# Kernel tuning notes

Hardware: AMD Instinct MI355X
Metric: run time of the kernel (lower is better)

## Reference

```python
import jax, jax.numpy as jnp
import numpy as np

T = 2048        # flattened tokens (one prefill sequence)
HID = 2048      # hidden_size
NH = 32         # query heads
NKV = 4         # kv heads
HD = 128        # head_dim
THETA = 1000000.0
EPS = 1e-6


def setup_inputs() -> dict:
    key = jax.random.key(0)
    k0, k1, k2 = jax.random.split(key, 3)
    return {
        "positions": jnp.arange(T, dtype=jnp.int32),
        "hidden_states": jax.random.normal(k0, (T, HID), dtype=jnp.float32),
        "w_qkv": jax.random.normal(k1, ((NH + 2 * NKV) * HD, HID), dtype=jnp.float32) * 0.02,
        "w_o": jax.random.normal(k2, (HID, NH * HD), dtype=jnp.float32) * 0.02,
        "q_norm_w": jnp.ones((HD,), dtype=jnp.float32),
        "k_norm_w": jnp.ones((HD,), dtype=jnp.float32),
    }


def _rmsnorm(x, w):
    # per-head RMSNorm over last dim (head_dim), fp32 math
    var = jnp.mean(x * x, axis=-1, keepdims=True)
    return x * jax.lax.rsqrt(var + EPS) * w


def _rope(x, positions):
    # NeoX-style rotary embedding over full head_dim
    d = x.shape[-1]
    inv_freq = 1.0 / (THETA ** (jnp.arange(0, d, 2, dtype=jnp.float32) / d))  # [d/2]
    ang = positions.astype(jnp.float32)[:, None] * inv_freq                   # [T, d/2]
    cos = jnp.cos(ang)[:, None, :]  # [T,1,d/2]
    sin = jnp.sin(ang)[:, None, :]
    x1, x2 = jnp.split(x, 2, axis=-1)
    return jnp.concatenate([x1 * cos - x2 * sin, x2 * cos + x1 * sin], axis=-1)


def reference(positions, hidden_states, w_qkv, w_o, q_norm_w, k_norm_w):
    # fused QKV projection (no bias)
    qkv = hidden_states @ w_qkv.T                       # [T, (NH+2*NKV)*HD]
    q, k, v = jnp.split(qkv, [NH * HD, (NH + NKV) * HD], axis=-1)
    q = _rmsnorm(q.reshape(T, NH, HD), q_norm_w)        # [T,NH,HD]
    k = _rmsnorm(k.reshape(T, NKV, HD), k_norm_w)       # [T,NKV,HD]
    v = v.reshape(T, NKV, HD)
    q = _rope(q, positions)
    k = _rope(k, positions)
    # GQA: expand kv heads to query heads
    g = NH // NKV
    k = jnp.repeat(k, g, axis=1)                        # [T,NH,HD]
    v = jnp.repeat(v, g, axis=1)
    scale = HD ** -0.5
    scores = jnp.einsum('qhd,khd->hqk', q, k) * scale   # [NH,T,T]
    causal = jnp.tril(jnp.ones((T, T), dtype=bool))
    scores = jnp.where(causal[None, :, :], scores, jnp.finfo(scores.dtype).min)
    attn = jax.nn.softmax(scores, axis=-1)
    o = jnp.einsum('hqk,khd->qhd', attn, v).reshape(T, NH * HD)
    return o @ w_o.T                                    # [T,HID]
```

## Files before the change

### kernel.cpp

```cpp
#include <hip/hip_runtime.h>
#include <math.h>

#define T 2048
#define HID 2048
#define NH 32
#define NKV 4
#define HD 128
#define QKV_DIM 5120
#define OD 4096
#define C2LOG 0.12751743f
#define MFIX 6.0f

typedef _Float16 half8 __attribute__((ext_vector_type(8)));
typedef _Float16 half4v __attribute__((ext_vector_type(4)));
typedef float floatx4 __attribute__((ext_vector_type(4)));

#define GLD16(gp, lp) __builtin_amdgcn_global_load_lds( \
    (const __attribute__((address_space(1))) void*)(gp), \
    (__attribute__((address_space(3))) void*)(lp), 16, 0, 0)

__global__ __launch_bounds__(256)
void cvt_f16(const float* __restrict__ in, _Float16* __restrict__ out, int n) {
    int i = (blockIdx.x * 256 + threadIdx.x) * 4;
    if (i < n) {
        float4 v = *(const float4*)(in + i);
        half4v o = { (_Float16)v.x, (_Float16)v.y, (_Float16)v.z, (_Float16)v.w };
        *(half4v*)(out + i) = o;
    }
}

__global__ void init_cnt(unsigned* c) { if (threadIdx.x == 0) *c = 0u; }

__global__ __launch_bounds__(256)
void gemm_nt(const _Float16* __restrict__ A, const _Float16* __restrict__ B,
             float* __restrict__ C, int M, int N, int K) {
    __shared__ __align__(16) _Float16 Asm[4096];
    __shared__ __align__(16) _Float16 Bsm[4096];
    int tid = threadIdx.x;
    int wave = tid >> 6, lane = tid & 63;
    int quad = lane >> 4, l16 = lane & 15;
    int m0 = blockIdx.y * 128, n0 = blockIdx.x * 128;
    int wm = (wave >> 1) * 64, wn = (wave & 1) * 64;
    const _Float16* Ag = A + (size_t)(m0 + (tid >> 2)) * K + (tid & 3) * 8;
    const _Float16* Bg = B + (size_t)(n0 + (tid >> 2)) * K + (tid & 3) * 8;
    size_t row64 = (size_t)64 * K;
    _Float16* AsmW = Asm + wave * 512;
    _Float16* BsmW = Bsm + wave * 512;
    floatx4 acc[4][4] = {};
    for (int k0 = 0; k0 < K; k0 += 32) {
        __syncthreads();
        GLD16(Ag + k0, AsmW);
        GLD16(Ag + row64 + k0, AsmW + 2048);
        GLD16(Bg + k0, BsmW);
        GLD16(Bg + row64 + k0, BsmW + 2048);
        __syncthreads();
        half8 af[4], bf[4];
        #pragma unroll
        for (int i = 0; i < 4; i++)
            af[i] = *(const half8*)&Asm[(wm + i * 16 + l16) * 32 + quad * 8];
        #pragma unroll
        for (int j = 0; j < 4; j++)
            bf[j] = *(const half8*)&Bsm[(wn + j * 16 + l16) * 32 + quad * 8];
        #pragma unroll
        for (int i = 0; i < 4; i++)
            #pragma unroll
            for (int j = 0; j < 4; j++)
                acc[i][j] = __builtin_amdgcn_mfma_f32_16x16x32_f16(af[i], bf[j], acc[i][j], 0, 0, 0);
    }
    #pragma unroll
    for (int i = 0; i < 4; i++) {
        int row = m0 + wm + i * 16 + quad * 4;
        #pragma unroll
        for (int j = 0; j < 4; j++) {
            int col = n0 + wn + j * 16 + l16;
            #pragma unroll
            for (int r = 0; r < 4; r++)
                C[(size_t)(row + r) * N + col] = acc[i][j][r];
        }
    }
}

__global__ __launch_bounds__(256)
void gemm_nt_64(const _Float16* __restrict__ A, const _Float16* __restrict__ B,
                float* __restrict__ C, int M, int N, int K) {
    __shared__ __align__(16) _Float16 Asm[4096];
    __shared__ __align__(16) _Float16 Bsm[2048];
    int tid = threadIdx.x;
    int wave = tid >> 6, lane = tid & 63;
    int quad = lane >> 4, l16 = lane & 15;
    int m0 = blockIdx.y * 128, n0 = blockIdx.x * 64;
    int wm = wave * 32;
    const _Float16* Ag = A + (size_t)(m0 + (tid >> 2)) * K + (tid & 3) * 8;
    const _Float16* Bg = B + (size_t)(n0 + (tid >> 2)) * K + (tid & 3) * 8;
    size_t row64 = (size_t)64 * K;
    _Float16* AsmW = Asm + wave * 512;
    _Float16* BsmW = Bsm + wave * 512;
    floatx4 acc[2][4] = {};
    for (int k0 = 0; k0 < K; k0 += 32) {
        __syncthreads();
        GLD16(Ag + k0, AsmW);
        GLD16(Ag + row64 + k0, AsmW + 2048);
        GLD16(Bg + k0, BsmW);
        __syncthreads();
        half8 af[2], bf[4];
        #pragma unroll
        for (int i = 0; i < 2; i++)
            af[i] = *(const half8*)&Asm[(wm + i * 16 + l16) * 32 + quad * 8];
        #pragma unroll
        for (int j = 0; j < 4; j++)
            bf[j] = *(const half8*)&Bsm[(j * 16 + l16) * 32 + quad * 8];
        #pragma unroll
        for (int i = 0; i < 2; i++)
            #pragma unroll
            for (int j = 0; j < 4; j++)
                acc[i][j] = __builtin_amdgcn_mfma_f32_16x16x32_f16(af[i], bf[j], acc[i][j], 0, 0, 0);
    }
    #pragma unroll
    for (int i = 0; i < 2; i++) {
        int row = m0 + wm + i * 16 + quad * 4;
        #pragma unroll
        for (int j = 0; j < 4; j++) {
            int col = n0 + j * 16 + l16;
            #pragma unroll
            for (int r = 0; r < 4; r++)
                C[(size_t)(row + r) * N + col] = acc[i][j][r];
        }
    }
}

__global__ __launch_bounds__(256)
void qkv_post(const float* __restrict__ qkv, const int* __restrict__ positions,
              const float* __restrict__ qw, const float* __restrict__ kw,
              _Float16* __restrict__ Qb, _Float16* __restrict__ Kb,
              _Float16* __restrict__ Vt) {
    int t = blockIdx.x;
    int wave = threadIdx.x >> 6, lane = threadIdx.x & 63;
    float pos = (float)positions[t];
    float f = exp2f(-(float)lane * (19.9315685693241741f / 64.0f));
    float ang = pos * f;
    float s = sinf(ang), c = cosf(ang);
    const float* row = qkv + (size_t)t * QKV_DIM;
    for (int hh = wave; hh < NH + 2 * NKV; hh += 4) {
        float x1 = row[hh * HD + lane];
        float x2 = row[hh * HD + lane + 64];
        if (hh < NH + NKV) {
            float ss = x1 * x1 + x2 * x2;
            for (int o = 1; o < 64; o <<= 1) ss += __shfl_xor(ss, o);
            float inv = rsqrtf(ss * (1.0f / HD) + 1e-6f);
            const float* w = (hh < NH) ? qw : kw;
            x1 = x1 * inv * w[lane];
            x2 = x2 * inv * w[lane + 64];
            float y1 = x1 * c - x2 * s;
            float y2 = x2 * c + x1 * s;
            _Float16* dst;
            if (hh < NH) dst = Qb + ((size_t)hh * T + t) * HD;
            else         dst = Kb + ((size_t)(hh - NH) * T + t) * HD;
            dst[lane]      = (_Float16)y1;
            dst[lane + 64] = (_Float16)y2;
        } else {
            int hk = hh - NH - NKV;
            Vt[((size_t)hk * HD + lane) * T + t]      = (_Float16)x1;
            Vt[((size_t)hk * HD + lane + 64) * T + t] = (_Float16)x2;
        }
    }
}

__global__ __launch_bounds__(256)
void attn(const _Float16* __restrict__ Qb, const _Float16* __restrict__ Kb,
          const _Float16* __restrict__ Vt, _Float16* __restrict__ Ob,
          unsigned* __restrict__ cnt) {
    __shared__ __align__(16) _Float16 Ksm[8192];
    __shared__ __align__(16) _Float16 Vsm[8192];
    __shared__ __align__(16) _Float16 Psm[4][16][72];
    __shared__ unsigned item_s;
    int tid = threadIdx.x, wave = tid >> 6, lane = tid & 63;
    int quad = lane >> 4, l16 = lane & 15;

    for (;;) {
        if (tid == 0) item_s = atomicAdd(cnt, 1u);
        __syncthreads();
        unsigned item = item_s;
        if (item >= 512u) break;
        int h = (int)(item & 31u);
        int qt = 15 - (int)(item >> 5);
        int hk = h >> 3;
        int q0 = qt * 128;
        int wbase = q0 + wave * 32;

        half8 aq[2][4];
        #pragma unroll
        for (int g = 0; g < 2; g++) {
            int qrow = wbase + g * 16 + l16;
            const _Float16* qp = Qb + ((size_t)h * T + qrow) * HD + quad * 8;
            #pragma unroll
            for (int dk = 0; dk < 4; dk++)
                aq[g][dk] = *(const half8*)(qp + dk * 32);
        }
        floatx4 o_acc[2][8] = {};
        float lpart[2][4] = {};

        int krow = tid >> 4;
        const _Float16* Kg = Kb + ((size_t)hk * T + krow) * HD + ((tid & 15) ^ (krow & 7)) * 8;
        int vrow = tid >> 3;
        const _Float16* Vg = Vt + ((size_t)hk * HD + vrow) * T + ((tid & 7) ^ (vrow & 7)) * 8;
        _Float16* KsmW = Ksm + wave * 512;
        _Float16* VsmW = Vsm + wave * 512;

        int ntiles = 2 * qt + 2;
        for (int it = 0; it < ntiles; it++) {
            int kv0 = it * 64;
            __syncthreads();
            {
                const _Float16* kg = Kg + (size_t)kv0 * HD;
                const _Float16* vg = Vg + kv0;
                #pragma unroll
                for (int c = 0; c < 4; c++) {
                    GLD16(kg + (size_t)c * (16 * HD), KsmW + c * 2048);
                    GLD16(vg + (size_t)c * (32 * T), VsmW + c * 2048);
                }
            }
            __syncthreads();
            if (kv0 > wbase + 31) continue;

            floatx4 sfr[2][4];
            #pragma unroll
            for (int sn = 0; sn < 4; sn++) {
                int row = sn * 16 + l16;
                int rs = row & 7;
                half8 kf[4];
                #pragma unroll
                for (int dk = 0; dk < 4; dk++)
                    kf[dk] = *(const half8*)&Ksm[row * 128 + ((dk * 4 + quad) ^ rs) * 8];
                #pragma unroll
                for (int g = 0; g < 2; g++) {
                    floatx4 a = {};
                    #pragma unroll
                    for (int dk = 0; dk < 4; dk++)
                        a = __builtin_amdgcn_mfma_f32_16x16x32_f16(aq[g][dk], kf[dk], a, 0, 0, 0);
                    sfr[g][sn] = a;
                }
            }

            bool act[2];
            half8 ap[2][2];
            #pragma unroll
            for (int g = 0; g < 2; g++) {
                int bg = wbase + g * 16;
                act[g] = (kv0 <= bg + 15);
                if (!act[g]) continue;
                bool needmask = (kv0 + 63 > bg);
                int rq = bg + quad * 4;
                #pragma unroll
                for (int sn = 0; sn < 4; sn++) {
                    int kv = kv0 + sn * 16 + l16;
                    #pragma unroll
                    for (int r = 0; r < 4; r++) {
                        float p = __builtin_amdgcn_exp2f(
                            __builtin_fmaf(sfr[g][sn][r], C2LOG, -MFIX));
                        if (needmask) p = (kv <= rq + r) ? p : 0.0f;
                        lpart[g][r] += p;
                        Psm[wave][quad * 4 + r][sn * 16 + l16] = (_Float16)p;
                    }
                }
                ap[g][0] = *(const half8*)&Psm[wave][l16][quad * 8];
                ap[g][1] = *(const half8*)&Psm[wave][l16][32 + quad * 8];
            }

            #pragma unroll
            for (int dn = 0; dn < 8; dn++) {
                int row = dn * 16 + l16;
                int rs = row & 7;
                half8 v0 = *(const half8*)&Vsm[row * 64 + ((quad ^ rs) * 8)];
                half8 v1 = *(const half8*)&Vsm[row * 64 + (((4 + quad) ^ rs) * 8)];
                #pragma unroll
                for (int g = 0; g < 2; g++) {
                    if (!act[g]) continue;
                    o_acc[g][dn] = __builtin_amdgcn_mfma_f32_16x16x32_f16(ap[g][0], v0, o_acc[g][dn], 0, 0, 0);
                    o_acc[g][dn] = __builtin_amdgcn_mfma_f32_16x16x32_f16(ap[g][1], v1, o_acc[g][dn], 0, 0, 0);
                }
            }
        }

        #pragma unroll
        for (int g = 0; g < 2; g++) {
            #pragma unroll
            for (int o = 1; o < 16; o <<= 1)
                #pragma unroll
                for (int r = 0; r < 4; r++)
                    lpart[g][r] += __shfl_xor(lpart[g][r], o);
            float linv[4];
            #pragma unroll
            for (int r = 0; r < 4; r++) linv[r] = 1.0f / lpart[g][r];
            int rowb = wbase + g * 16 + quad * 4;
            #pragma unroll
            for (int dn = 0; dn < 8; dn++) {
                int col = h * HD + dn * 16 + l16;
                #pragma unroll
                for (int r = 0; r < 4; r++)
                    Ob[(size_t)(rowb + r) * OD + col] = (_Float16)(o_acc[g][dn][r] * linv[r]);
            }
        }
    }
}

extern "C" void kernel_launch(void* const* d_in, const int* in_sizes, int n_in,
                              void* d_out, int out_size, void* d_ws, size_t ws_size,
                              hipStream_t stream) {
    const int*   positions = (const int*)d_in[0];
    const float* hidden    = (const float*)d_in[1];
    const float* w_qkv     = (const float*)d_in[2];
    const float* w_o       = (const float*)d_in[3];
    const float* q_norm_w  = (const float*)d_in[4];
    const float* k_norm_w  = (const float*)d_in[5];
    float* out = (float*)d_out;

    char* ws = (char*)d_ws;
    _Float16* hb    = (_Float16*)(ws);
    _Float16* wqkvb = (_Float16*)(ws + 8388608);
    _Float16* wob   = (_Float16*)(ws + 29360128);
    float*    qkvf  = (float*)   (ws + 46137344);
    _Float16* Qb    = (_Float16*)(ws + 88080384);
    _Float16* Kb    = (_Float16*)(ws + 104857600);
    _Float16* Vt    = (_Float16*)(ws + 106954752);
    _Float16* Ob    = (_Float16*)(ws + 109051904);
    unsigned* cnt   = (unsigned*)(ws + 125829120);

    cvt_f16<<<(T * HID / 4 + 255) / 256, 256, 0, stream>>>(hidden, hb, T * HID);
    cvt_f16<<<(QKV_DIM * HID / 4 + 255) / 256, 256, 0, stream>>>(w_qkv, wqkvb, QKV_DIM * HID);
    cvt_f16<<<(HID * OD / 4 + 255) / 256, 256, 0, stream>>>(w_o, wob, HID * OD);

    gemm_nt<<<dim3(QKV_DIM / 128, T / 128), 256, 0, stream>>>(hb, wqkvb, qkvf, T, QKV_DIM, HID);

    qkv_post<<<T, 256, 0, stream>>>(qkvf, positions, q_norm_w, k_norm_w, Qb, Kb, Vt);

    init_cnt<<<1, 64, 0, stream>>>(cnt);
    attn<<<768, 256, 0, stream>>>(Qb, Kb, Vt, Ob, cnt);

    gemm_nt_64<<<dim3(HID / 64, T / 128), 256, 0, stream>>>(Ob, wob, out, T, HID, OD);
}
```

Before: 379.5 us.

## Restructure attention to static 64-row tiles, fuse conversions, store QKV in fp16

The attention kernel drops the atomic work-queue with 128-row query tiles and uses a static grid of 1024 blocks, each handling a 64-row query tile. Blocks are ordered to pair long and short causal tiles, and the P staging buffer gets an XOR swizzle. The three fp32-to-fp16 conversion kernels become one launch, and the counter-init launch is removed. The QKV GEMM now writes fp16 instead of fp32, halving intermediate traffic at the cost of rounding QKV before RMSNorm.

Result: faster. 350.0 us (-7.8%).

```diff
diff --git a/kernel.cpp b/kernel.cpp
--- a/kernel.cpp
+++ b/kernel.cpp
@@ -20,20 +20,23 @@
     (__attribute__((address_space(3))) void*)(lp), 16, 0, 0)
 
 __global__ __launch_bounds__(256)
-void cvt_f16(const float* __restrict__ in, _Float16* __restrict__ out, int n) {
-    int i = (blockIdx.x * 256 + threadIdx.x) * 4;
-    if (i < n) {
-        float4 v = *(const float4*)(in + i);
-        half4v o = { (_Float16)v.x, (_Float16)v.y, (_Float16)v.z, (_Float16)v.w };
-        *(half4v*)(out + i) = o;
-    }
-}
-
-__global__ void init_cnt(unsigned* c) { if (threadIdx.x == 0) *c = 0u; }
+void cvt_all(const float* __restrict__ h, const float* __restrict__ wq,
+             const float* __restrict__ wo, _Float16* __restrict__ out) {
+    size_t i = ((size_t)blockIdx.x * 256 + threadIdx.x) * 4;
+    const float* src;
+    size_t off;
+    if (i < (size_t)T * HID)                        { src = h;  off = i; }
+    else if (i < (size_t)T * HID + (size_t)QKV_DIM * HID)
+                                                    { src = wq; off = i - (size_t)T * HID; }
+    else                                            { src = wo; off = i - (size_t)T * HID - (size_t)QKV_DIM * HID; }
+    float4 v = *(const float4*)(src + off);
+    half4v o = { (_Float16)v.x, (_Float16)v.y, (_Float16)v.z, (_Float16)v.w };
+    *(half4v*)(out + i) = o;
+}
 
 __global__ __launch_bounds__(256)
-void gemm_nt(const _Float16* __restrict__ A, const _Float16* __restrict__ B,
-             float* __restrict__ C, int M, int N, int K) {
+void gemm_nt_h(const _Float16* __restrict__ A, const _Float16* __restrict__ B,
+               _Float16* __restrict__ C, int M, int N, int K) {
     __shared__ __align__(16) _Float16 Asm[4096];
     __shared__ __align__(16) _Float16 Bsm[4096];
     int tid = threadIdx.x;
@@ -75,7 +78,7 @@
             int col = n0 + wn + j * 16 + l16;
             #pragma unroll
             for (int r = 0; r < 4; r++)
-                C[(size_t)(row + r) * N + col] = acc[i][j][r];
+                C[(size_t)(row + r) * N + col] = (_Float16)acc[i][j][r];
         }
     }
 }
@@ -129,7 +132,7 @@
 }
 
 __global__ __launch_bounds__(256)
-void qkv_post(const float* __restrict__ qkv, const int* __restrict__ positions,
+void qkv_post(const _Float16* __restrict__ qkv, const int* __restrict__ positions,
               const float* __restrict__ qw, const float* __restrict__ kw,
               _Float16* __restrict__ Qb, _Float16* __restrict__ Kb,
               _Float16* __restrict__ Vt) {
@@ -139,10 +142,10 @@
     float f = exp2f(-(float)lane * (19.9315685693241741f / 64.0f));
     float ang = pos * f;
     float s = sinf(ang), c = cosf(ang);
-    const float* row = qkv + (size_t)t * QKV_DIM;
+    const _Float16* row = qkv + (size_t)t * QKV_DIM;
     for (int hh = wave; hh < NH + 2 * NKV; hh += 4) {
-        float x1 = row[hh * HD + lane];
-        float x2 = row[hh * HD + lane + 64];
+        float x1 = (float)row[hh * HD + lane];
+        float x2 = (float)row[hh * HD + lane + 64];
         if (hh < NH + NKV) {
             float ss = x1 * x1 + x2 * x2;
             for (int o = 1; o < 64; o <<= 1) ss += __shfl_xor(ss, o);
@@ -165,141 +168,116 @@
     }
 }
 
-__global__ __launch_bounds__(256)
+__global__ __launch_bounds__(256, 4)
 void attn(const _Float16* __restrict__ Qb, const _Float16* __restrict__ Kb,
-          const _Float16* __restrict__ Vt, _Float16* __restrict__ Ob,
-          unsigned* __restrict__ cnt) {
+          const _Float16* __restrict__ Vt, _Float16* __restrict__ Ob) {
     __shared__ __align__(16) _Float16 Ksm[8192];
     __shared__ __align__(16) _Float16 Vsm[8192];
-    __shared__ __align__(16) _Float16 Psm[4][16][72];
-    __shared__ unsigned item_s;
+    __shared__ __align__(16) _Float16 Psm[4][1024];
+    int b = blockIdx.x;
+    int h = b & 31;
+    int quarter = b >> 8;
+    int i = (b & 255) >> 5;
+    int qt = (quarter == 0) ? 31 - i : (quarter == 1) ? i
+           : (quarter == 2) ? 23 - i : 8 + i;
+    int hk = h >> 3;
     int tid = threadIdx.x, wave = tid >> 6, lane = tid & 63;
     int quad = lane >> 4, l16 = lane & 15;
-
-    for (;;) {
-        if (tid == 0) item_s = atomicAdd(cnt, 1u);
-        __syncthreads();
-        unsigned item = item_s;
-        if (item >= 512u) break;
-        int h = (int)(item & 31u);
-        int qt = 15 - (int)(item >> 5);
-        int hk = h >> 3;
-        int q0 = qt * 128;
-        int wbase = q0 + wave * 32;
-
-        half8 aq[2][4];
-        #pragma unroll
-        for (int g = 0; g < 2; g++) {
-            int qrow = wbase + g * 16 + l16;
-            const _Float16* qp = Qb + ((size_t)h * T + qrow) * HD + quad * 8;
-            #pragma unroll
-            for (int dk = 0; dk < 4; dk++)
-                aq[g][dk] = *(const half8*)(qp + dk * 32);
-        }
-        floatx4 o_acc[2][8] = {};
-        float lpart[2][4] = {};
-
-        int krow = tid >> 4;
-        const _Float16* Kg = Kb + ((size_t)hk * T + krow) * HD + ((tid & 15) ^ (krow & 7)) * 8;
-        int vrow = tid >> 3;
-        const _Float16* Vg = Vt + ((size_t)hk * HD + vrow) * T + ((tid & 7) ^ (vrow & 7)) * 8;
-        _Float16* KsmW = Ksm + wave * 512;
-        _Float16* VsmW = Vsm + wave * 512;
-
-        int ntiles = 2 * qt + 2;
-        for (int it = 0; it < ntiles; it++) {
-            int kv0 = it * 64;
-            __syncthreads();
-            {
-                const _Float16* kg = Kg + (size_t)kv0 * HD;
-                const _Float16* vg = Vg + kv0;
-                #pragma unroll
-                for (int c = 0; c < 4; c++) {
-                    GLD16(kg + (size_t)c * (16 * HD), KsmW + c * 2048);
-                    GLD16(vg + (size_t)c * (32 * T), VsmW + c * 2048);
-                }
+    int q0 = qt * 64;
+    int wbase = q0 + wave * 16;
+
+    half8 aq[4];
+    {
+        const _Float16* qp = Qb + ((size_t)h * T + wbase + l16) * HD + quad * 8;
+        #pragma unroll
+        for (int dk = 0; dk < 4; dk++)
+            aq[dk] = *(const half8*)(qp + dk * 32);
+    }
+    floatx4 o_acc[8] = {};
+    float lpart[4] = {};
+
+    int krow = tid >> 4;
+    const _Float16* Kg = Kb + ((size_t)hk * T + krow) * HD + ((tid & 15) ^ (krow & 7)) * 8;
+    int vrow = tid >> 3;
+    const _Float16* Vg = Vt + ((size_t)hk * HD + vrow) * T + ((tid & 7) ^ (vrow & 7)) * 8;
+    _Float16* KsmW = Ksm + wave * 512;
+    _Float16* VsmW = Vsm + wave * 512;
+    _Float16* PsmW = Psm[wave];
+
+    int ntiles = qt + 1;
+    for (int it = 0; it < ntiles; it++) {
+        int kv0 = it * 64;
+        __syncthreads();
+        {
+            const _Float16* kg = Kg + (size_t)kv0 * HD;
+            const _Float16* vg = Vg + kv0;
+            #pragma unroll
+            for (int c = 0; c < 4; c++) {
+                GLD16(kg + (size_t)c * (16 * HD), KsmW + c * 2048);
+                GLD16(vg + (size_t)c * (32 * T), VsmW + c * 2048);
             }
-            __syncthreads();
-            if (kv0 > wbase + 31) continue;
-
-            floatx4 sfr[2][4];
-            #pragma unroll
-            for (int sn = 0; sn < 4; sn++) {
-                int row = sn * 16 + l16;
-                int rs = row & 7;
-                half8 kf[4];
-                #pragma unroll
-                for (int dk = 0; dk < 4; dk++)
-                    kf[dk] = *(const half8*)&Ksm[row * 128 + ((dk * 4 + quad) ^ rs) * 8];
-                #pragma unroll
-                for (int g = 0; g < 2; g++) {
-                    floatx4 a = {};
-                    #pragma unroll
-                    for (int dk = 0; dk < 4; dk++)
-                        a = __builtin_amdgcn_mfma_f32_16x16x32_f16(aq[g][dk], kf[dk], a, 0, 0, 0);
-                    sfr[g][sn] = a;
-                }
+        }
+        __syncthreads();
+
+        floatx4 sfr[4];
+        #pragma unroll
+        for (int sn = 0; sn < 4; sn++) {
+            int row = sn * 16 + l16;
+            int rs = row & 7;
+            floatx4 a = {};
+            #pragma unroll
+            for (int dk = 0; dk < 4; dk++) {
+                half8 kf = *(const half8*)&Ksm[row * 128 + ((dk * 4 + quad) ^ rs) * 8];
+                a = __builtin_amdgcn_mfma_f32_16x16x32_f16(aq[dk], kf, a, 0, 0, 0);
             }
-
-            bool act[2];
-            half8 ap[2][2];
-            #pragma unroll
-            for (int g = 0; g < 2; g++) {
-                int bg = wbase + g * 16;
-                act[g] = (kv0 <= bg + 15);
-                if (!act[g]) continue;
-                bool needmask = (kv0 + 63 > bg);
-                int rq = bg + quad * 4;
-                #pragma unroll
-                for (int sn = 0; sn < 4; sn++) {
-                    int kv = kv0 + sn * 16 + l16;
-                    #pragma unroll
-                    for (int r = 0; r < 4; r++) {
-                        float p = __builtin_amdgcn_exp2f(
-                            __builtin_fmaf(sfr[g][sn][r], C2LOG, -MFIX));
-                        if (needmask) p = (kv <= rq + r) ? p : 0.0f;
-                        lpart[g][r] += p;
-                        Psm[wave][quad * 4 + r][sn * 16 + l16] = (_Float16)p;
-                    }
-                }
-                ap[g][0] = *(const half8*)&Psm[wave][l16][quad * 8];
-                ap[g][1] = *(const half8*)&Psm[wave][l16][32 + quad * 8];
+            sfr[sn] = a;
+        }
+
+        bool needmask = (it == ntiles - 1);
+        int rq = wbase + quad * 4;
+        #pragma unroll
+        for (int sn = 0; sn < 4; sn++) {
+            int kv = kv0 + sn * 16 + l16;
+            #pragma unroll
+            for (int r = 0; r < 4; r++) {
+                float p = __builtin_amdgcn_exp2f(
+                    __builtin_fmaf(sfr[sn][r], C2LOG, -MFIX));
+                if (needmask) p = (kv <= rq + r) ? p : 0.0f;
+                lpart[r] += p;
+                int prow = quad * 4 + r;
+                int cb = sn * 2 + (l16 >> 3);
+                PsmW[prow * 64 + ((cb ^ (prow & 7)) * 8 + (l16 & 7))] = (_Float16)p;
             }
-
-            #pragma unroll
-            for (int dn = 0; dn < 8; dn++) {
-                int row = dn * 16 + l16;
-                int rs = row & 7;
-                half8 v0 = *(const half8*)&Vsm[row * 64 + ((quad ^ rs) * 8)];
-                half8 v1 = *(const half8*)&Vsm[row * 64 + (((4 + quad) ^ rs) * 8)];
-                #pragma unroll
-                for (int g = 0; g < 2; g++) {
-                    if (!act[g]) continue;
-                    o_acc[g][dn] = __builtin_amdgcn_mfma_f32_16x16x32_f16(ap[g][0], v0, o_acc[g][dn], 0, 0, 0);
-                    o_acc[g][dn] = __builtin_amdgcn_mfma_f32_16x16x32_f16(ap[g][1], v1, o_acc[g][dn], 0, 0, 0);
-                }
-            }
-        }
-
-        #pragma unroll
-        for (int g = 0; g < 2; g++) {
-            #pragma unroll
-            for (int o = 1; o < 16; o <<= 1)
-                #pragma unroll
-                for (int r = 0; r < 4; r++)
-                    lpart[g][r] += __shfl_xor(lpart[g][r], o);
-            float linv[4];
-            #pragma unroll
-            for (int r = 0; r < 4; r++) linv[r] = 1.0f / lpart[g][r];
-            int rowb = wbase + g * 16 + quad * 4;
-            #pragma unroll
-            for (int dn = 0; dn < 8; dn++) {
-                int col = h * HD + dn * 16 + l16;
-                #pragma unroll
-                for (int r = 0; r < 4; r++)
-                    Ob[(size_t)(rowb + r) * OD + col] = (_Float16)(o_acc[g][dn][r] * linv[r]);
-            }
-        }
+        }
+        half8 ap0 = *(const half8*)&PsmW[l16 * 64 + ((quad ^ (l16 & 7)) * 8)];
+        half8 ap1 = *(const half8*)&PsmW[l16 * 64 + (((4 + quad) ^ (l16 & 7)) * 8)];
+
+        #pragma unroll
+        for (int dn = 0; dn < 8; dn++) {
+            int row = dn * 16 + l16;
+            int rs = row & 7;
+            half8 v0 = *(const half8*)&Vsm[row * 64 + ((quad ^ rs) * 8)];
+            half8 v1 = *(const half8*)&Vsm[row * 64 + (((4 + quad) ^ rs) * 8)];
+            o_acc[dn] = __builtin_amdgcn_mfma_f32_16x16x32_f16(ap0, v0, o_acc[dn], 0, 0, 0);
+            o_acc[dn] = __builtin_amdgcn_mfma_f32_16x16x32_f16(ap1, v1, o_acc[dn], 0, 0, 0);
+        }
+    }
+
+    #pragma unroll
+    for (int o = 1; o < 16; o <<= 1)
+        #pragma unroll
+        for (int r = 0; r < 4; r++)
+            lpart[r] += __shfl_xor(lpart[r], o);
+    float linv[4];
+    #pragma unroll
+    for (int r = 0; r < 4; r++) linv[r] = 1.0f / lpart[r];
+    int rowb = wbase + quad * 4;
+    #pragma unroll
+    for (int dn = 0; dn < 8; dn++) {
+        int col = h * HD + dn * 16 + l16;
+        #pragma unroll
+        for (int r = 0; r < 4; r++)
+            Ob[(size_t)(rowb + r) * OD + col] = (_Float16)(o_acc[dn][r] * linv[r]);
     }
 }
 
@@ -318,23 +296,19 @@
     _Float16* hb    = (_Float16*)(ws);
     _Float16* wqkvb = (_Float16*)(ws + 8388608);
     _Float16* wob   = (_Float16*)(ws + 29360128);
-    float*    qkvf  = (float*)   (ws + 46137344);
+    _Float16* qkvh  = (_Float16*)(ws + 46137344);
     _Float16* Qb    = (_Float16*)(ws + 88080384);
     _Float16* Kb    = (_Float16*)(ws + 104857600);
     _Float16* Vt    = (_Float16*)(ws + 106954752);
     _Float16* Ob    = (_Float16*)(ws + 109051904);
-    unsigned* cnt   = (unsigned*)(ws + 125829120);
-
-    cvt_f16<<<(T * HID / 4 + 255) / 256, 256, 0, stream>>>(hidden, hb, T * HID);
-    cvt_f16<<<(QKV_DIM * HID / 4 + 255) / 256, 256, 0, stream>>>(w_qkv, wqkvb, QKV_DIM * HID);
-    cvt_f16<<<(HID * OD / 4 + 255) / 256, 256, 0, stream>>>(w_o, wob, HID * OD);
-
-    gemm_nt<<<dim3(QKV_DIM / 128, T / 128), 256, 0, stream>>>(hb, wqkvb, qkvf, T, QKV_DIM, HID);
-
-    qkv_post<<<T, 256, 0, stream>>>(qkvf, positions, q_norm_w, k_norm_w, Qb, Kb, Vt);
-
-    init_cnt<<<1, 64, 0, stream>>>(cnt);
-    attn<<<768, 256, 0, stream>>>(Qb, Kb, Vt, Ob, cnt);
+
+    cvt_all<<<22528, 256, 0, stream>>>(hidden, w_qkv, w_o, hb);
+
+    gemm_nt_h<<<dim3(QKV_DIM / 128, T / 128), 256, 0, stream>>>(hb, wqkvb, qkvh, T, QKV_DIM, HID);
+
+    qkv_post<<<T, 256, 0, stream>>>(qkvh, positions, q_norm_w, k_norm_w, Qb, Kb, Vt);
+
+    attn<<<1024, 256, 0, stream>>>(Qb, Kb, Vt, Ob);
 
     gemm_nt_64<<<dim3(HID / 64, T / 128), 256, 0, stream>>>(Ob, wob, out, T, HID, OD);
 }
```
